# Kernel tuning notes

Measured on AMD Instinct MI355X. Metric: run time of the kernel, lower is better.

Reference implementation:

```python
import jax, jax.numpy as jnp
import numpy as np

T, B, U = 64, 2048, 1024


def setup_inputs() -> dict:
    key = jax.random.key(0)
    ks = jax.random.split(key, 7)
    inputs = jax.random.normal(ks[0], (T, B, 1), dtype=jnp.float32)
    x1_0 = jax.random.normal(ks[1], (B, 1), dtype=jnp.float32)
    x2_0 = jax.random.normal(ks[2], (B, 1), dtype=jnp.float32)
    c0 = jax.random.normal(ks[3], (B, U), dtype=jnp.float32)
    kernel = jax.random.normal(ks[4], (1, 2 * U), dtype=jnp.float32) * 0.05
    # orthogonal-ish recurrent kernel, scaled for stability
    recurrent_kernel = jax.random.normal(ks[5], (U, 2 * U), dtype=jnp.float32) * (1.0 / np.sqrt(U))
    # unit_forget_bias: ones for the f gate, zeros for the c gate
    bias = jnp.concatenate([jnp.ones((U,), jnp.float32), jnp.zeros((U,), jnp.float32)])
    output_kernel = jax.random.normal(ks[6], (U, 1), dtype=jnp.float32) * 0.05
    return {"inputs": inputs, "x1_0": x1_0, "x2_0": x2_0, "c0": c0,
            "kernel": kernel, "recurrent_kernel": recurrent_kernel,
            "bias": bias, "output_kernel": output_kernel}


def reference(inputs, x1_0, x2_0, c0, kernel, recurrent_kernel, bias, output_kernel):
    U = c0.shape[-1]
    Kf, Kc = kernel[:, :U], kernel[:, U:2 * U]          # [1,U] each
    Rf, Rc = recurrent_kernel[:, :U], recurrent_kernel[:, U:2 * U]  # [U,U]
    bf, bc = bias[:U], bias[U:2 * U]

    def step(carry, inp):
        x1, x2, h = carry                 # x1,x2: [B,1]; h (= c_{t-1}): [B,U]
        x_f = h @ Rf + x1 @ Kf + bf       # [B,U]
        x_c = h @ Rc + x1 @ Kc + bc       # [B,U]
        f = jax.nn.sigmoid(x_f)
        c = f * h + (1.0 - f) * jnp.tanh(x_c)
        x1_new = x1 + x2                  # double-integrator position update
        x2_new = x2 + inp * (c @ output_kernel)  # velocity driven by scalar input * readout
        return (x1_new, x2_new, c), x1_new

    _, outputs = jax.lax.scan(step, (x1_0, x2_0, c0), inputs)
    return outputs  # [T, B, 1]
```

## Files before the change

### kernel.cpp

```cpp
#include <hip/hip_runtime.h>
#include <hip/hip_bf16.h>

#define T_STEPS 64
#define B_DIM 2048
#define U_DIM 1024

#define BM 128
#define BU 64
#define BK 64
#define KITERS (U_DIM / BK)

typedef __attribute__((ext_vector_type(8))) _Float16 h8;
typedef __attribute__((ext_vector_type(4))) float f4;

__device__ __forceinline__ void async_cp16(const _Float16* g, _Float16* l) {
    __builtin_amdgcn_global_load_lds((const __attribute__((address_space(1))) void*)g,
                                     (__attribute__((address_space(3))) void*)l,
                                     16, 0, 0);
}


__global__ void transpose_R(const float* __restrict__ R, _Float16* __restrict__ Rt) {
    __shared__ float tile[32][33];
    int nb = blockIdx.x * 32;
    int kb = blockIdx.y * 32;
    int tx = threadIdx.x, ty = threadIdx.y;
    #pragma unroll
    for (int i = ty; i < 32; i += 8)
        tile[i][tx] = R[(size_t)(kb + i) * (2 * U_DIM) + nb + tx];
    __syncthreads();
    #pragma unroll
    for (int i = ty; i < 32; i += 8)
        Rt[(size_t)(nb + i) * U_DIM + kb + tx] = (_Float16)tile[tx][i];
}

__global__ void init_state(const float* __restrict__ c0, _Float16* __restrict__ h0,
                           float* __restrict__ y) {
    int i = blockIdx.x * 256 + threadIdx.x;
    h0[i] = (_Float16)c0[i];
    if (i < 3 * B_DIM) y[i] = 0.f;
}

__global__ __launch_bounds__(256) void gemm_step(
    const _Float16* __restrict__ hA, _Float16* __restrict__ hB,
    const _Float16* __restrict__ Rt,
    const float* __restrict__ x1_0, const float* __restrict__ x2_0,
    float* __restrict__ x1w,
    float* __restrict__ x2w,
    const float* __restrict__ kern, const float* __restrict__ bias,
    const float* __restrict__ okern,
    float* __restrict__ y,
    const float* __restrict__ inputs,
    float* __restrict__ out,
    int t)
{
    __shared__ __align__(16) _Float16 lA [3][BM * BK];
    __shared__ __align__(16) _Float16 lBf[3][BU * BK];
    __shared__ __align__(16) _Float16 lBc[3][BU * BK];
    __shared__ __align__(16) _Float16 lC[BM * 72];
    __shared__ float x1s[BM];

    const int tid    = threadIdx.x;
    const int wid    = tid >> 6;
    const int lane   = tid & 63;
    const int lane15 = lane & 15;
    const int quad   = lane >> 4;
    const int u0     = blockIdx.x * BU;
    const int b0     = blockIdx.y * BM;
    const int wrow   = (wid >> 1) * 64;
    const int wcol   = (wid & 1) * 32;

    const int srow8 = lane >> 3;
    const int skc   = (lane & 7) ^ srow8;

    const _Float16* gA0  = hA + (size_t)(b0 + srow8) * U_DIM + skc * 8;
    const _Float16* gBf0 = Rt + (size_t)(u0 + srow8) * U_DIM + skc * 8;
    const _Float16* gBc0 = Rt + (size_t)(U_DIM + u0 + srow8) * U_DIM + skc * 8;

    auto stage = [&](int buf, int kt) {
        const int k0 = kt * BK;
        #pragma unroll
        for (int j = 0; j < 4; ++j) {
            const int r = wid * 4 + j;
            async_cp16(gA0 + (size_t)r * 8 * U_DIM + k0, &lA[buf][r * 512]);
        }
        #pragma unroll
        for (int j = 0; j < 2; ++j) {
            const int r = wid * 2 + j;
            async_cp16(gBf0 + (size_t)r * 8 * U_DIM + k0, &lBf[buf][r * 512]);
            async_cp16(gBc0 + (size_t)r * 8 * U_DIM + k0, &lBc[buf][r * 512]);
        }
    };

    stage(0, 0);
    stage(1, 1);

    if (tid < BM) {
        const int b = b0 + tid;
        float x1n, x2n;
        if (t == 0) {
            x1n = x1_0[b];
            x2n = x2_0[b];
        } else {
            const int rd = (t + 1) & 1;
            const float x1p = x1w[rd * B_DIM + b];
            const float x2p = x2w[rd * B_DIM + b];
            const float yp  = y[((t + 2) % 3) * B_DIM + b];
            const float ip  = inputs[(size_t)(t - 1) * B_DIM + b];
            x1n = x1p + x2p;
            x2n = x2p + ip * yp;
        }
        x1s[tid] = x1n;
        if (u0 == 0) {
            const int wr = t & 1;
            x1w[wr * B_DIM + b] = x1n;
            x2w[wr * B_DIM + b] = x2n;
            if (t > 0) out[(size_t)(t - 1) * B_DIM + b] = x1n;
            y[((t + 1) % 3) * B_DIM + b] = 0.f;
        }
    }

    f4 accF[4][2], accC[4][2];
    #pragma unroll
    for (int mt = 0; mt < 4; ++mt)
        #pragma unroll
        for (int nt = 0; nt < 2; ++nt) {
            accF[mt][nt] = (f4){0.f, 0.f, 0.f, 0.f};
            accC[mt][nt] = (f4){0.f, 0.f, 0.f, 0.f};
        }

    const int axor = lane15 & 7;

    for (int kt = 0; kt < KITERS; ++kt) {
        const int cur = kt % 3;
        if (kt < KITERS - 1)
            __builtin_amdgcn_s_waitcnt(0x0F78);
        else
            __builtin_amdgcn_s_waitcnt(0x0F70);
        __syncthreads();
        if (kt + 2 < KITERS) stage((kt + 2) % 3, kt + 2);

        #pragma unroll
        for (int ks = 0; ks < 2; ++ks) {
            h8 af[4], bff[2], bfc[2];
            #pragma unroll
            for (int mt = 0; mt < 4; ++mt) {
                const int row = wrow + mt * 16 + lane15;
                const int kq  = ks * 4 + quad;
                af[mt] = *(const h8*)&lA[cur][(row * 8 + (kq ^ axor)) * 8];
            }
            #pragma unroll
            for (int nt = 0; nt < 2; ++nt) {
                const int row = wcol + nt * 16 + lane15;
                const int kq  = ks * 4 + quad;
                bff[nt] = *(const h8*)&lBf[cur][(row * 8 + (kq ^ axor)) * 8];
                bfc[nt] = *(const h8*)&lBc[cur][(row * 8 + (kq ^ axor)) * 8];
            }
            #pragma unroll
            for (int mt = 0; mt < 4; ++mt)
                #pragma unroll
                for (int nt = 0; nt < 2; ++nt) {
                    accF[mt][nt] = __builtin_amdgcn_mfma_f32_16x16x32_f16(af[mt], bff[nt], accF[mt][nt], 0, 0, 0);
                    accC[mt][nt] = __builtin_amdgcn_mfma_f32_16x16x32_f16(af[mt], bfc[nt], accC[mt][nt], 0, 0, 0);
                }
        }
    }

    __syncthreads();
    {
        const int kh = u0 >> 6;
        const int k0 = kh * BK;
        #pragma unroll
        for (int j = 0; j < 4; ++j) {
            const int r = wid * 4 + j;
            async_cp16(gA0 + (size_t)r * 8 * U_DIM + k0, &lA[0][r * 512]);
        }
    }
    __builtin_amdgcn_s_waitcnt(0x0F70);
    __syncthreads();

    float* ycur = y + (t % 3) * B_DIM;
    #pragma unroll
    for (int mt = 0; mt < 4; ++mt) {
        const int rl_base = wrow + mt * 16 + quad * 4;
        float psum[4] = {0.f, 0.f, 0.f, 0.f};
        #pragma unroll
        for (int nt = 0; nt < 2; ++nt) {
            const int ul = wcol + nt * 16 + lane15;
            const int u  = u0 + ul;
            const float kf  = kern[u];
            const float kc  = kern[U_DIM + u];
            const float bfv = bias[u];
            const float bcv = bias[U_DIM + u];
            const float ok  = okern[u];
            #pragma unroll
            for (int reg = 0; reg < 4; ++reg) {
                const int rl = rl_base + reg;
                const float x1 = x1s[rl];
                const float xf = accF[mt][nt][reg] + x1 * kf + bfv;
                const float xc = accC[mt][nt][reg] + x1 * kc + bcv;
                const float fg = 1.f / (1.f + __expf(-xf));
                const float th = 1.f - 2.f / (1.f + __expf(2.f * xc));
                const float hv = (float)lA[0][(rl >> 3) * 512 +
                                              ((rl & 7) * 8 + ((ul >> 3) ^ (rl & 7))) * 8 +
                                              (ul & 7)];
                const float cv = fg * hv + (1.f - fg) * th;
                lC[rl * 72 + ul] = (_Float16)cv;
                psum[reg] += cv * ok;
            }
        }
        #pragma unroll
        for (int reg = 0; reg < 4; ++reg) {
            float s = psum[reg];
            s += __shfl_xor(s, 1);
            s += __shfl_xor(s, 2);
            s += __shfl_xor(s, 4);
            s += __shfl_xor(s, 8);
            if (lane15 == 0) atomicAdd(&ycur[b0 + rl_base + reg], s);
        }
    }

    __syncthreads();
    #pragma unroll
    for (int j = 0; j < 4; ++j) {
        const int idx = j * 256 + tid;
        const int row = idx >> 3;
        const int col = idx & 7;
        const uint4 v = *(const uint4*)&lC[row * 72 + col * 8];
        *(uint4*)&hB[(size_t)(b0 + row) * U_DIM + u0 + col * 8] = v;
    }
}

__global__ void finish(const float* __restrict__ x1w1, const float* __restrict__ x2w1,
                       float* __restrict__ out_last) {
    const int i = blockIdx.x * 256 + threadIdx.x;
    out_last[i] = x1w1[i] + x2w1[i];
}

extern "C" void kernel_launch(void* const* d_in, const int* in_sizes, int n_in,
                              void* d_out, int out_size, void* d_ws, size_t ws_size,
                              hipStream_t stream) {
    const float* inputs = (const float*)d_in[0];
    const float* x1_0   = (const float*)d_in[1];
    const float* x2_0   = (const float*)d_in[2];
    const float* c0     = (const float*)d_in[3];
    const float* kern   = (const float*)d_in[4];
    const float* rker   = (const float*)d_in[5];
    const float* bias   = (const float*)d_in[6];
    const float* okern  = (const float*)d_in[7];
    float* out = (float*)d_out;

    _Float16* Rt = (_Float16*)d_ws;
    _Float16* h0 = Rt + (size_t)2 * U_DIM * U_DIM;
    _Float16* h1 = h0 + (size_t)B_DIM * U_DIM;
    float* y   = (float*)(h1 + (size_t)B_DIM * U_DIM);
    float* x1w = y + 3 * B_DIM;
    float* x2w = x1w + 2 * B_DIM;

    transpose_R<<<dim3(64, 32), dim3(32, 8), 0, stream>>>(rker, Rt);
    init_state<<<dim3(B_DIM * U_DIM / 256), dim3(256), 0, stream>>>(c0, h0, y);

    _Float16* hcur = h0;
    _Float16* hnxt = h1;
    for (int t = 0; t < T_STEPS; ++t) {
        gemm_step<<<dim3(U_DIM / BU, B_DIM / BM), dim3(256), 0, stream>>>(
            hcur, hnxt, Rt, x1_0, x2_0, x1w, x2w, kern, bias, okern, y,
            inputs, out, t);
        _Float16* tmp = hcur; hcur = hnxt; hnxt = tmp;
    }
    finish<<<dim3(B_DIM / 256), dim3(256), 0, stream>>>(
        x1w + B_DIM, x2w + B_DIM, out + (size_t)(T_STEPS - 1) * B_DIM);
}
```

Before: 1.580 ms.

## Keep full-K recurrent weight slab in LDS and stream h from global into registers

The per-step GEMM tile changes to 256 batch rows by 32 units. Each block now loads its full-K slice of the f and c recurrent weights into padded LDS once, instead of pipelining K-tiles of both operands through triple-buffered LDS. The A operand (h) is read directly from global memory into registers with one-step prefetch, and the previous-h tile for the gate update is fetched asynchronously into a small LDS buffer that is also reused for the output staging. This removes the per-K-tile barriers and waits, but every wave now loads A through uncoalesced-ish global reads. LDS use rises to about 130KB, which allows only one block per CU (launch_bounds(256,1)), and the grid layout changes to match.

```diff
diff --git a/kernel.cpp b/kernel.cpp
--- a/kernel.cpp
+++ b/kernel.cpp
@@ -5,10 +5,11 @@
 #define B_DIM 2048
 #define U_DIM 1024
 
-#define BM 128
-#define BU 64
-#define BK 64
+#define BM 256
+#define BU 32
+#define BK 32
 #define KITERS (U_DIM / BK)
+#define BSTR 1032
 
 typedef __attribute__((ext_vector_type(8))) _Float16 h8;
 typedef __attribute__((ext_vector_type(4))) float f4;
@@ -41,7 +42,7 @@
     if (i < 3 * B_DIM) y[i] = 0.f;
 }
 
-__global__ __launch_bounds__(256) void gemm_step(
+__global__ __launch_bounds__(256, 1) void gemm_step(
     const _Float16* __restrict__ hA, _Float16* __restrict__ hB,
     const _Float16* __restrict__ Rt,
     const float* __restrict__ x1_0, const float* __restrict__ x2_0,
@@ -54,10 +55,8 @@
     float* __restrict__ out,
     int t)
 {
-    __shared__ __align__(16) _Float16 lA [3][BM * BK];
-    __shared__ __align__(16) _Float16 lBf[3][BU * BK];
-    __shared__ __align__(16) _Float16 lBc[3][BU * BK];
-    __shared__ __align__(16) _Float16 lC[BM * 72];
+    __shared__ __align__(16) _Float16 lB[2][BU * BSTR];
+    __shared__ __align__(16) _Float16 lH[BM * BU];
     __shared__ float x1s[BM];
 
     const int tid    = threadIdx.x;
@@ -65,37 +64,22 @@
     const int lane   = tid & 63;
     const int lane15 = lane & 15;
     const int quad   = lane >> 4;
-    const int u0     = blockIdx.x * BU;
+    const int ublk   = blockIdx.x;
+    const int u0     = ublk * BU;
     const int b0     = blockIdx.y * BM;
-    const int wrow   = (wid >> 1) * 64;
-    const int wcol   = (wid & 1) * 32;
-
-    const int srow8 = lane >> 3;
-    const int skc   = (lane & 7) ^ srow8;
-
-    const _Float16* gA0  = hA + (size_t)(b0 + srow8) * U_DIM + skc * 8;
-    const _Float16* gBf0 = Rt + (size_t)(u0 + srow8) * U_DIM + skc * 8;
-    const _Float16* gBc0 = Rt + (size_t)(U_DIM + u0 + srow8) * U_DIM + skc * 8;
-
-    auto stage = [&](int buf, int kt) {
-        const int k0 = kt * BK;
-        #pragma unroll
-        for (int j = 0; j < 4; ++j) {
-            const int r = wid * 4 + j;
-            async_cp16(gA0 + (size_t)r * 8 * U_DIM + k0, &lA[buf][r * 512]);
-        }
-        #pragma unroll
-        for (int j = 0; j < 2; ++j) {
-            const int r = wid * 2 + j;
-            async_cp16(gBf0 + (size_t)r * 8 * U_DIM + k0, &lBf[buf][r * 512]);
-            async_cp16(gBc0 + (size_t)r * 8 * U_DIM + k0, &lBc[buf][r * 512]);
-        }
-    };
-
-    stage(0, 0);
-    stage(1, 1);
-
-    if (tid < BM) {
+    const int wrow   = wid * 64;
+
+    #pragma unroll 8
+    for (int i = 0; i < 32; ++i) {
+        const int idx = i * 256 + tid;
+        const int c   = idx & 127;
+        const int r   = (idx >> 7) & 31;
+        const int hf  = idx >> 12;
+        const h8 v = *(const h8*)&Rt[(size_t)(hf * U_DIM + u0 + r) * U_DIM + c * 8];
+        *(h8*)&lB[hf][r * BSTR + c * 8] = v;
+    }
+
+    {
         const int b = b0 + tid;
         float x1n, x2n;
         if (t == 0) {
@@ -111,7 +95,7 @@
             x2n = x2p + ip * yp;
         }
         x1s[tid] = x1n;
-        if (u0 == 0) {
+        if (ublk == 0) {
             const int wr = t & 1;
             x1w[wr * B_DIM + b] = x1n;
             x2w[wr * B_DIM + b] = x2n;
@@ -120,6 +104,27 @@
         }
     }
 
+    float kf[2], kc[2], bf_[2], bc_[2], ok_[2];
+    #pragma unroll
+    for (int nt = 0; nt < 2; ++nt) {
+        const int u = u0 + nt * 16 + lane15;
+        kf[nt] = kern[u];
+        kc[nt] = kern[U_DIM + u];
+        bf_[nt] = bias[u];
+        bc_[nt] = bias[U_DIM + u];
+        ok_[nt] = okern[u];
+    }
+
+    #pragma unroll
+    for (int j = 0; j < 4; ++j) {
+        const int r = wid * 4 + j;
+        const _Float16* g = hA + (size_t)(b0 + r * 16 + (lane >> 2)) * U_DIM
+                               + u0 + (lane & 3) * 8;
+        async_cp16(g, &lH[r * 512]);
+    }
+
+    __syncthreads();
+
     f4 accF[4][2], accC[4][2];
     #pragma unroll
     for (int mt = 0; mt < 4; ++mt)
@@ -129,84 +134,59 @@
             accC[mt][nt] = (f4){0.f, 0.f, 0.f, 0.f};
         }
 
-    const int axor = lane15 & 7;
-
+    h8 a[2][4];
+    #pragma unroll
+    for (int mt = 0; mt < 4; ++mt)
+        a[0][mt] = *(const h8*)&hA[(size_t)(b0 + wrow + mt * 16 + lane15) * U_DIM + quad * 8];
+
+    #pragma unroll 2
     for (int kt = 0; kt < KITERS; ++kt) {
-        const int cur = kt % 3;
-        if (kt < KITERS - 1)
-            __builtin_amdgcn_s_waitcnt(0x0F78);
-        else
-            __builtin_amdgcn_s_waitcnt(0x0F70);
-        __syncthreads();
-        if (kt + 2 < KITERS) stage((kt + 2) % 3, kt + 2);
-
-        #pragma unroll
-        for (int ks = 0; ks < 2; ++ks) {
-            h8 af[4], bff[2], bfc[2];
+        if (kt + 1 < KITERS) {
+            const size_t k0 = (size_t)(kt + 1) * BK + quad * 8;
             #pragma unroll
-            for (int mt = 0; mt < 4; ++mt) {
-                const int row = wrow + mt * 16 + lane15;
-                const int kq  = ks * 4 + quad;
-                af[mt] = *(const h8*)&lA[cur][(row * 8 + (kq ^ axor)) * 8];
-            }
+            for (int mt = 0; mt < 4; ++mt)
+                a[(kt + 1) & 1][mt] =
+                    *(const h8*)&hA[(size_t)(b0 + wrow + mt * 16 + lane15) * U_DIM + k0];
+        }
+        h8 bff[2], bcc[2];
+        #pragma unroll
+        for (int nt = 0; nt < 2; ++nt) {
+            const int off = (nt * 16 + lane15) * BSTR + kt * BK + quad * 8;
+            bff[nt] = *(const h8*)&lB[0][off];
+            bcc[nt] = *(const h8*)&lB[1][off];
+        }
+        #pragma unroll
+        for (int mt = 0; mt < 4; ++mt)
             #pragma unroll
             for (int nt = 0; nt < 2; ++nt) {
-                const int row = wcol + nt * 16 + lane15;
-                const int kq  = ks * 4 + quad;
-                bff[nt] = *(const h8*)&lBf[cur][(row * 8 + (kq ^ axor)) * 8];
-                bfc[nt] = *(const h8*)&lBc[cur][(row * 8 + (kq ^ axor)) * 8];
+                accF[mt][nt] = __builtin_amdgcn_mfma_f32_16x16x32_f16(a[kt & 1][mt], bff[nt], accF[mt][nt], 0, 0, 0);
+                accC[mt][nt] = __builtin_amdgcn_mfma_f32_16x16x32_f16(a[kt & 1][mt], bcc[nt], accC[mt][nt], 0, 0, 0);
             }
-            #pragma unroll
-            for (int mt = 0; mt < 4; ++mt)
-                #pragma unroll
-                for (int nt = 0; nt < 2; ++nt) {
-                    accF[mt][nt] = __builtin_amdgcn_mfma_f32_16x16x32_f16(af[mt], bff[nt], accF[mt][nt], 0, 0, 0);
-                    accC[mt][nt] = __builtin_amdgcn_mfma_f32_16x16x32_f16(af[mt], bfc[nt], accC[mt][nt], 0, 0, 0);
-                }
-        }
-    }
-
-    __syncthreads();
-    {
-        const int kh = u0 >> 6;
-        const int k0 = kh * BK;
-        #pragma unroll
-        for (int j = 0; j < 4; ++j) {
-            const int r = wid * 4 + j;
-            async_cp16(gA0 + (size_t)r * 8 * U_DIM + k0, &lA[0][r * 512]);
-        }
-    }
+    }
+
     __builtin_amdgcn_s_waitcnt(0x0F70);
     __syncthreads();
 
     float* ycur = y + (t % 3) * B_DIM;
     #pragma unroll
     for (int mt = 0; mt < 4; ++mt) {
-        const int rl_base = wrow + mt * 16 + quad * 4;
+        const int rlb = wrow + mt * 16 + quad * 4;
         float psum[4] = {0.f, 0.f, 0.f, 0.f};
         #pragma unroll
         for (int nt = 0; nt < 2; ++nt) {
-            const int ul = wcol + nt * 16 + lane15;
-            const int u  = u0 + ul;
-            const float kf  = kern[u];
-            const float kc  = kern[U_DIM + u];
-            const float bfv = bias[u];
-            const float bcv = bias[U_DIM + u];
-            const float ok  = okern[u];
+            const int ul = nt * 16 + lane15;
             #pragma unroll
             for (int reg = 0; reg < 4; ++reg) {
-                const int rl = rl_base + reg;
+                const int rl = rlb + reg;
                 const float x1 = x1s[rl];
-                const float xf = accF[mt][nt][reg] + x1 * kf + bfv;
-                const float xc = accC[mt][nt][reg] + x1 * kc + bcv;
+                const float xf = accF[mt][nt][reg] + x1 * kf[nt] + bf_[nt];
+                const float xc = accC[mt][nt][reg] + x1 * kc[nt] + bc_[nt];
                 const float fg = 1.f / (1.f + __expf(-xf));
                 const float th = 1.f - 2.f / (1.f + __expf(2.f * xc));
-                const float hv = (float)lA[0][(rl >> 3) * 512 +
-                                              ((rl & 7) * 8 + ((ul >> 3) ^ (rl & 7))) * 8 +
-                                              (ul & 7)];
+                const float hv = (float)lH[rl * BU + ul];
                 const float cv = fg * hv + (1.f - fg) * th;
-                lC[rl * 72 + ul] = (_Float16)cv;
-                psum[reg] += cv * ok;
+                lH[rl * BU + ul] = (_Float16)cv;
+                psum[reg] += cv * ok_[nt];
             }
         }
         #pragma unroll
@@ -216,7 +196,7 @@
             s += __shfl_xor(s, 2);
             s += __shfl_xor(s, 4);
             s += __shfl_xor(s, 8);
-            if (lane15 == 0) atomicAdd(&ycur[b0 + rl_base + reg], s);
+            if (lane15 == 0) atomicAdd(&ycur[b0 + rlb + reg], s);
         }
     }
 
@@ -224,10 +204,10 @@
     #pragma unroll
     for (int j = 0; j < 4; ++j) {
         const int idx = j * 256 + tid;
-        const int row = idx >> 3;
-        const int col = idx & 7;
-        const uint4 v = *(const uint4*)&lC[row * 72 + col * 8];
-        *(uint4*)&hB[(size_t)(b0 + row) * U_DIM + u0 + col * 8] = v;
+        const int row = idx >> 2;
+        const int c4  = idx & 3;
+        *(uint4*)&hB[(size_t)(b0 + row) * U_DIM + u0 + c4 * 8] =
+            *(const uint4*)&lH[row * BU + c4 * 8];
     }
 }
 
```

New measurement: 1.762 ms. +11.5%, slower.

## Shrink K tile and unify LDS staging to fit two blocks per CU

Applied to the files above, without the earlier changes.

Halves the K tile to 32 and merges the A, Bf, Bc and output tiles into one triple-buffered shared array that is reused for the epilogue, which roughly halves shared-memory use. Launch bounds now request two blocks per CU. The previous-state values used in the gate blend are loaded into registers before the main loop instead of being re-fetched into LDS afterwards, and the per-unit constants are hoisted. The aim is more resident blocks to hide latency, at the cost of twice as many barrier-synchronised K iterations and higher register pressure.

```diff
diff --git a/kernel.cpp b/kernel.cpp
--- a/kernel.cpp
+++ b/kernel.cpp
@@ -7,8 +7,10 @@
 
 #define BM 128
 #define BU 64
-#define BK 64
+#define BK 32
 #define KITERS (U_DIM / BK)
+#define NST 3
+#define STG 8192
 
 typedef __attribute__((ext_vector_type(8))) _Float16 h8;
 typedef __attribute__((ext_vector_type(4))) float f4;
@@ -41,7 +43,7 @@
     if (i < 3 * B_DIM) y[i] = 0.f;
 }
 
-__global__ __launch_bounds__(256) void gemm_step(
+__global__ __launch_bounds__(256, 2) void gemm_step(
     const _Float16* __restrict__ hA, _Float16* __restrict__ hB,
     const _Float16* __restrict__ Rt,
     const float* __restrict__ x1_0, const float* __restrict__ x2_0,
@@ -54,10 +56,7 @@
     float* __restrict__ out,
     int t)
 {
-    __shared__ __align__(16) _Float16 lA [3][BM * BK];
-    __shared__ __align__(16) _Float16 lBf[3][BU * BK];
-    __shared__ __align__(16) _Float16 lBc[3][BU * BK];
-    __shared__ __align__(16) _Float16 lC[BM * 72];
+    __shared__ __align__(16) _Float16 lS[NST][STG];
     __shared__ float x1s[BM];
 
     const int tid    = threadIdx.x;
@@ -69,31 +68,6 @@
     const int b0     = blockIdx.y * BM;
     const int wrow   = (wid >> 1) * 64;
     const int wcol   = (wid & 1) * 32;
-
-    const int srow8 = lane >> 3;
-    const int skc   = (lane & 7) ^ srow8;
-
-    const _Float16* gA0  = hA + (size_t)(b0 + srow8) * U_DIM + skc * 8;
-    const _Float16* gBf0 = Rt + (size_t)(u0 + srow8) * U_DIM + skc * 8;
-    const _Float16* gBc0 = Rt + (size_t)(U_DIM + u0 + srow8) * U_DIM + skc * 8;
-
-    auto stage = [&](int buf, int kt) {
-        const int k0 = kt * BK;
-        #pragma unroll
-        for (int j = 0; j < 4; ++j) {
-            const int r = wid * 4 + j;
-            async_cp16(gA0 + (size_t)r * 8 * U_DIM + k0, &lA[buf][r * 512]);
-        }
-        #pragma unroll
-        for (int j = 0; j < 2; ++j) {
-            const int r = wid * 2 + j;
-            async_cp16(gBf0 + (size_t)r * 8 * U_DIM + k0, &lBf[buf][r * 512]);
-            async_cp16(gBc0 + (size_t)r * 8 * U_DIM + k0, &lBc[buf][r * 512]);
-        }
-    };
-
-    stage(0, 0);
-    stage(1, 1);
 
     if (tid < BM) {
         const int b = b0 + tid;
@@ -111,7 +85,7 @@
             x2n = x2p + ip * yp;
         }
         x1s[tid] = x1n;
-        if (u0 == 0) {
+        if (blockIdx.x == 0) {
             const int wr = t & 1;
             x1w[wr * B_DIM + b] = x1n;
             x2w[wr * B_DIM + b] = x2n;
@@ -120,6 +94,44 @@
         }
     }
 
+    float kf[2], kc[2], bf_[2], bc_[2], ok_[2];
+    #pragma unroll
+    for (int nt = 0; nt < 2; ++nt) {
+        const int u = u0 + wcol + nt * 16 + lane15;
+        kf[nt] = kern[u];
+        kc[nt] = kern[U_DIM + u];
+        bf_[nt] = bias[u];
+        bc_[nt] = bias[U_DIM + u];
+        ok_[nt] = okern[u];
+    }
+    _Float16 hv[4][2][4];
+    #pragma unroll
+    for (int mt = 0; mt < 4; ++mt)
+        #pragma unroll
+        for (int nt = 0; nt < 2; ++nt)
+            #pragma unroll
+            for (int reg = 0; reg < 4; ++reg)
+                hv[mt][nt][reg] = hA[(size_t)(b0 + wrow + mt * 16 + quad * 4 + reg) * U_DIM
+                                     + u0 + wcol + nt * 16 + lane15];
+
+    const int srow  = lane >> 2;
+    const int schnk = ((lane & 3) ^ (srow & 3)) * 8;
+    auto stage = [&](int buf, int kt) {
+        const int k0 = kt * BK;
+        #pragma unroll
+        for (int j = 0; j < 2; ++j) {
+            const int r = wid * 2 + j;
+            async_cp16(hA + (size_t)(b0 + r * 16 + srow) * U_DIM + k0 + schnk,
+                       &lS[buf][r * 512]);
+        }
+        async_cp16(Rt + (size_t)(u0 + wid * 16 + srow) * U_DIM + k0 + schnk,
+                   &lS[buf][4096 + wid * 512]);
+        async_cp16(Rt + (size_t)(U_DIM + u0 + wid * 16 + srow) * U_DIM + k0 + schnk,
+                   &lS[buf][6144 + wid * 512]);
+    };
+    stage(0, 0);
+    stage(1, 1);
+
     f4 accF[4][2], accC[4][2];
     #pragma unroll
     for (int mt = 0; mt < 4; ++mt)
@@ -129,84 +141,60 @@
             accC[mt][nt] = (f4){0.f, 0.f, 0.f, 0.f};
         }
 
-    const int axor = lane15 & 7;
-
     for (int kt = 0; kt < KITERS; ++kt) {
         const int cur = kt % 3;
         if (kt < KITERS - 1)
-            __builtin_amdgcn_s_waitcnt(0x0F78);
+            __builtin_amdgcn_s_waitcnt(0x0F74);
         else
             __builtin_amdgcn_s_waitcnt(0x0F70);
         __syncthreads();
         if (kt + 2 < KITERS) stage((kt + 2) % 3, kt + 2);
 
-        #pragma unroll
-        for (int ks = 0; ks < 2; ++ks) {
-            h8 af[4], bff[2], bfc[2];
-            #pragma unroll
-            for (int mt = 0; mt < 4; ++mt) {
-                const int row = wrow + mt * 16 + lane15;
-                const int kq  = ks * 4 + quad;
-                af[mt] = *(const h8*)&lA[cur][(row * 8 + (kq ^ axor)) * 8];
-            }
+        h8 af[4], bff[2], bfc[2];
+        #pragma unroll
+        for (int mt = 0; mt < 4; ++mt) {
+            const int R = wrow + mt * 16 + lane15;
+            af[mt] = *(const h8*)&lS[cur][(R >> 4) * 512 + lane15 * 32 +
+                                          ((quad ^ (lane15 & 3)) * 8)];
+        }
+        #pragma unroll
+        for (int nt = 0; nt < 2; ++nt) {
+            const int Rb = wcol + nt * 16 + lane15;
+            const int off = (Rb >> 4) * 512 + lane15 * 32 + ((quad ^ (lane15 & 3)) * 8);
+            bff[nt] = *(const h8*)&lS[cur][4096 + off];
+            bfc[nt] = *(const h8*)&lS[cur][6144 + off];
+        }
+        #pragma unroll
+        for (int mt = 0; mt < 4; ++mt)
             #pragma unroll
             for (int nt = 0; nt < 2; ++nt) {
-                const int row = wcol + nt * 16 + lane15;
-                const int kq  = ks * 4 + quad;
-                bff[nt] = *(const h8*)&lBf[cur][(row * 8 + (kq ^ axor)) * 8];
-                bfc[nt] = *(const h8*)&lBc[cur][(row * 8 + (kq ^ axor)) * 8];
+                accF[mt][nt] = __builtin_amdgcn_mfma_f32_16x16x32_f16(af[mt], bff[nt], accF[mt][nt], 0, 0, 0);
+                accC[mt][nt] = __builtin_amdgcn_mfma_f32_16x16x32_f16(af[mt], bfc[nt], accC[mt][nt], 0, 0, 0);
             }
-            #pragma unroll
-            for (int mt = 0; mt < 4; ++mt)
-                #pragma unroll
-                for (int nt = 0; nt < 2; ++nt) {
-                    accF[mt][nt] = __builtin_amdgcn_mfma_f32_16x16x32_f16(af[mt], bff[nt], accF[mt][nt], 0, 0, 0);
-                    accC[mt][nt] = __builtin_amdgcn_mfma_f32_16x16x32_f16(af[mt], bfc[nt], accC[mt][nt], 0, 0, 0);
-                }
-        }
     }
 
     __syncthreads();
-    {
-        const int kh = u0 >> 6;
-        const int k0 = kh * BK;
-        #pragma unroll
-        for (int j = 0; j < 4; ++j) {
-            const int r = wid * 4 + j;
-            async_cp16(gA0 + (size_t)r * 8 * U_DIM + k0, &lA[0][r * 512]);
-        }
-    }
-    __builtin_amdgcn_s_waitcnt(0x0F70);
-    __syncthreads();
-
+
+    _Float16* lC = &lS[0][0];
     float* ycur = y + (t % 3) * B_DIM;
     #pragma unroll
     for (int mt = 0; mt < 4; ++mt) {
-        const int rl_base = wrow + mt * 16 + quad * 4;
+        const int rlb = wrow + mt * 16 + quad * 4;
         float psum[4] = {0.f, 0.f, 0.f, 0.f};
         #pragma unroll
         for (int nt = 0; nt < 2; ++nt) {
             const int ul = wcol + nt * 16 + lane15;
-            const int u  = u0 + ul;
-            const float kf  = kern[u];
-            const float kc  = kern[U_DIM + u];
-            const float bfv = bias[u];
-            const float bcv = bias[U_DIM + u];
-            const float ok  = okern[u];
             #pragma unroll
             for (int reg = 0; reg < 4; ++reg) {
-                const int rl = rl_base + reg;
+                const int rl = rlb + reg;
                 const float x1 = x1s[rl];
-                const float xf = accF[mt][nt][reg] + x1 * kf + bfv;
-                const float xc = accC[mt][nt][reg] + x1 * kc + bcv;
+                const float xf = accF[mt][nt][reg] + x1 * kf[nt] + bf_[nt];
+                const float xc = accC[mt][nt][reg] + x1 * kc[nt] + bc_[nt];
                 const float fg = 1.f / (1.f + __expf(-xf));
                 const float th = 1.f - 2.f / (1.f + __expf(2.f * xc));
-                const float hv = (float)lA[0][(rl >> 3) * 512 +
-                                              ((rl & 7) * 8 + ((ul >> 3) ^ (rl & 7))) * 8 +
-                                              (ul & 7)];
-                const float cv = fg * hv + (1.f - fg) * th;
+                const float cv = fg * (float)hv[mt][nt][reg] + (1.f - fg) * th;
                 lC[rl * 72 + ul] = (_Float16)cv;
-                psum[reg] += cv * ok;
+                psum[reg] += cv * ok_[nt];
             }
         }
         #pragma unroll
@@ -216,7 +204,7 @@
             s += __shfl_xor(s, 2);
             s += __shfl_xor(s, 4);
             s += __shfl_xor(s, 8);
-            if (lane15 == 0) atomicAdd(&ycur[b0 + rl_base + reg], s);
+            if (lane15 == 0) atomicAdd(&ycur[b0 + rlb + reg], s);
         }
     }
 
@@ -226,8 +214,8 @@
         const int idx = j * 256 + tid;
         const int row = idx >> 3;
         const int col = idx & 7;
-        const uint4 v = *(const uint4*)&lC[row * 72 + col * 8];
-        *(uint4*)&hB[(size_t)(b0 + row) * U_DIM + u0 + col * 8] = v;
+        *(uint4*)&hB[(size_t)(b0 + row) * U_DIM + u0 + col * 8] =
+            *(const uint4*)&lC[row * 72 + col * 8];
     }
 }
 
```

Result: faster. 1.536 ms (-2.8%).
